# Kernel tuning notes

Measured on AMD Instinct MI355X. Metric: run time of the kernel, lower is better.

## Reference

```python
import jax, jax.numpy as jnp
import numpy as np

B, N, DIM = 2, 2048, 512
H, DH = 8, 64
INNER = H * DH
SCALE = DH ** -0.5


def setup_inputs() -> dict:
    key = jax.random.key(0)
    ks = jax.random.split(key, 8)
    s = 0.02
    return {
        "nodes": jax.random.normal(ks[0], (B, N, DIM), dtype=jnp.float32),
        "edge_mask": jax.random.bernoulli(ks[1], 0.9, (B, N, N)),
        "wq": jax.random.normal(ks[2], (DIM, INNER), dtype=jnp.float32) * s,
        "bq": jnp.zeros((INNER,), dtype=jnp.float32),
        "wkv": jax.random.normal(ks[3], (DIM, 2 * INNER), dtype=jnp.float32) * s,
        "bkv": jnp.zeros((2 * INNER,), dtype=jnp.float32),
        "wo": jax.random.normal(ks[4], (INNER, DIM), dtype=jnp.float32) * s,
        "bo": jnp.zeros((DIM,), dtype=jnp.float32),
    }


def reference(nodes, edge_mask, wq, bq, wkv, bkv, wo, bo):
    b, n, _ = nodes.shape
    q = nodes @ wq + bq                      # [b, n, h*dh]
    kv = nodes @ wkv + bkv                   # [b, n, 2*h*dh]
    k, v = jnp.split(kv, 2, axis=-1)
    # split heads -> [b, h, n, dh]
    split = lambda t: t.reshape(b, n, H, DH).transpose(0, 2, 1, 3)
    q, k, v = split(q), split(k), split(v)
    sim = jnp.einsum('bhid,bhjd->bhij', q, k) * SCALE
    max_neg = -jnp.finfo(sim.dtype).max
    sim = jnp.where(edge_mask[:, None, :, :], sim, max_neg)
    attn = jax.nn.softmax(sim, axis=-1)
    out = jnp.einsum('bhij,bhjd->bhid', attn, v)      # [b, h, n, dh]
    out = out.transpose(0, 2, 1, 3).reshape(b, n, INNER)
    return out @ wo + bo
```

## Files before the change

### kernel.cpp

```cpp
#include <hip/hip_runtime.h>
#include <cstdint>
#include <cstddef>

#define DEVI __device__ __forceinline__

typedef __bf16 bf16x8 __attribute__((ext_vector_type(8)));
typedef float floatx4 __attribute__((ext_vector_type(4)));
typedef unsigned short us4v __attribute__((ext_vector_type(4)));
typedef unsigned short us8 __attribute__((ext_vector_type(8)));

static_assert(sizeof(bf16x8) == 16, "bf16x8 must be 16B");
static_assert(sizeof(us8) == 16, "us8 must be 16B");


#if __has_builtin(__builtin_amdgcn_cvt_pk_bf16_f32)
DEVI unsigned short f2bf(float f) {
  typedef __bf16 bf16x2 __attribute__((ext_vector_type(2)));
  union { bf16x2 v; unsigned short u[2]; } c;
  c.v = __builtin_amdgcn_cvt_pk_bf16_f32(f, 0.f);
  return c.u[0];
}
#else
DEVI unsigned short f2bf(float f) {
  unsigned int u = __float_as_uint(f);
  u += 0x7fffu + ((u >> 16) & 1u);
  return (unsigned short)(u >> 16);
}
#endif

DEVI float exp2c(float x) {
#if __has_builtin(__builtin_amdgcn_exp2f)
  return __builtin_amdgcn_exp2f(x);
#else
  return exp2f(x);
#endif
}

DEVI bf16x8 ld8(const unsigned short* p) { return *(const bf16x8*)p; }

typedef const __attribute__((address_space(1))) void* gas_ptr;
typedef __attribute__((address_space(3))) void* las_ptr;

DEVI void gld16(const void* g, void* l) {
  __builtin_amdgcn_global_load_lds((gas_ptr)g, (las_ptr)l, 16, 0, 0);
}

#define WAIT_LGKM0() __builtin_amdgcn_s_waitcnt(0xc07f)
#define WAIT_VM12()  __builtin_amdgcn_s_waitcnt(0x0f7c)
#define WAIT_VM0()   __builtin_amdgcn_s_waitcnt(0x0f70)
#define SB()         __builtin_amdgcn_sched_barrier(0)

__global__ __launch_bounds__(256) void prep_k(
    const float* __restrict__ nodes, const void* __restrict__ mask,
    const float* __restrict__ wq, const float* __restrict__ wkv,
    const float* __restrict__ wo,
    unsigned short* __restrict__ XB, unsigned short* __restrict__ WQKVT,
    unsigned short* __restrict__ WOT, unsigned int* __restrict__ pm) {
  int bid = blockIdx.x;
  if (bid < 8192) {
    __shared__ int mode;
    const unsigned int* md = (const unsigned int*)mask;
    unsigned int probe = md[threadIdx.x];
    bool odd = (probe > 1u && probe != 0x3f800000u);
    if (threadIdx.x == 0) mode = 0;
    __syncthreads();
    if (odd) atomicOr(&mode, 1);
    __syncthreads();
    int byteMode = mode;
    int t = bid * 256 + threadIdx.x;
    int lane = threadIdx.x & 63;
    unsigned int n;
    if (byteMode) {
      unsigned int x = md[t];
      n = ((x & 0xffu) ? 1u : 0u) | ((x & 0xff00u) ? 2u : 0u) |
          ((x & 0xff0000u) ? 4u : 0u) | ((x >> 24) ? 8u : 0u);
    } else {
      uint4 v = ((const uint4*)mask)[t];
      n = (v.x ? 1u : 0u) | (v.y ? 2u : 0u) | (v.z ? 4u : 0u) | (v.w ? 8u : 0u);
    }
    unsigned int w = n << ((lane & 7) * 4);
    w |= __shfl_xor(w, 1);
    w |= __shfl_xor(w, 2);
    w |= __shfl_xor(w, 4);
    if ((lane & 7) == 0) pm[t >> 3] = w;
  } else if (bid < 10240) {
    int i = (bid - 8192) * 256 + threadIdx.x;
    float4 v = ((const float4*)nodes)[i];
    us4v o;
    o[0] = f2bf(v.x); o[1] = f2bf(v.y); o[2] = f2bf(v.z); o[3] = f2bf(v.w);
    *(us4v*)(XB + (size_t)i * 4) = o;
  } else {
    int tb = bid - 10240;
    int x = tb & 15, y = (tb >> 4) & 7, z = tb >> 7;
    const float* src; unsigned short* dst; int C, c0;
    if (z == 0)      { if (x >= 8) return; src = wq;  dst = WQKVT; C = 512;  c0 = 0; }
    else if (z == 1) { src = wkv; dst = WQKVT; C = 1024; c0 = 512; }
    else             { if (x >= 8) return; src = wo;  dst = WOT;  C = 512;  c0 = 0; }
    __shared__ unsigned short t2[64 * 64];
    const int t = threadIdx.x;
    const int ct = x * 64, rt = y * 64;
    for (int p = 0; p < 4; p++) {
      int kl = p * 16 + (t >> 4);
      int cc = (t & 15) * 4;
      float4 v = *(const float4*)&src[(size_t)(rt + kl) * C + ct + cc];
      float f[4] = {v.x, v.y, v.z, v.w};
      for (int i = 0; i < 4; i++) {
        int c = cc + i;
        t2[c * 64 + (kl ^ (c & 56))] = f2bf(f[i]);
      }
    }
    __syncthreads();
    for (int p = 0; p < 2; p++) {
      int c = p * 32 + (t >> 3);
      int kc = (t & 7) * 8;
      us8 v = *(const us8*)&t2[c * 64 + (kc ^ (c & 56))];
      *(us8*)&dst[(size_t)(c0 + ct + c) * 512 + rt + kc] = v;
    }
  }
}

__global__ __launch_bounds__(256) void gemm_qkv_k(
    const unsigned short* __restrict__ A,
    const unsigned short* __restrict__ Bt,
    const float* __restrict__ bq, const float* __restrict__ bkv,
    unsigned short* __restrict__ Qo, unsigned short* __restrict__ Ko,
    unsigned short* __restrict__ VTo) {
  __shared__ unsigned short smem[8192];
  unsigned short* sA = smem;
  unsigned short* sB = smem + 2048;
  const int tid = threadIdx.x;
  const int wave = tid >> 6, lane = tid & 63, quad = lane >> 4, l16 = lane & 15;
  const int wm = wave >> 1, wn = wave & 1;
  const int bm = blockIdx.x, bn = blockIdx.y;
  floatx4 acc[2][4] = {};
  const int arow = lane >> 2;
  const int ag = lane & 3;
  for (int kt = 0; kt < 16; kt++) {
    __syncthreads();
    {
      int rowA = wave * 16 + arow;
      int gA = ag ^ (rowA & 3);
      gld16(&A[(size_t)(bm * 64 + rowA) * 512 + kt * 32 + gA * 8], &sA[(wave * 16) * 32]);
      for (int p = 0; p < 2; p++) {
        int rowB = p * 64 + wave * 16 + arow;
        int gB = ag ^ (rowB & 3);
        gld16(&Bt[(size_t)(bn * 128 + rowB) * 512 + kt * 32 + gB * 8],
              &sB[(p * 64 + wave * 16) * 32]);
      }
    }
    __syncthreads();
    bf16x8 aF[2], bF[4];
    int swz = (quad ^ (l16 & 3)) * 8;
    for (int i = 0; i < 2; i++) aF[i] = ld8(&sA[(wm * 32 + i * 16 + l16) * 32 + swz]);
    for (int j = 0; j < 4; j++) bF[j] = ld8(&sB[(wn * 64 + j * 16 + l16) * 32 + swz]);
    for (int i = 0; i < 2; i++)
      for (int j = 0; j < 4; j++)
        acc[i][j] = __builtin_amdgcn_mfma_f32_16x16x32_bf16(aF[i], bF[j], acc[i][j], 0, 0, 0);
  }

  const int sec = bn * 2 + wn;
  float bias[4];
  float scale = 1.0f;
  if (sec < 8) {
    for (int j = 0; j < 4; j++) bias[j] = bq[sec * 64 + j * 16 + l16];
    scale = 0.18033688011112042f;
  } else {
    for (int j = 0; j < 4; j++) bias[j] = bkv[(sec - 8) * 64 + j * 16 + l16];
  }
  const int gr0 = bm * 64 + wm * 32;
  const int b = gr0 >> 11, n0 = gr0 & 2047;
  unsigned short* pw = smem + wave * 2048;
  __syncthreads();
  if (sec < 16) {
    for (int i = 0; i < 2; i++)
      for (int j = 0; j < 4; j++) {
        int cg = j * 2 + (l16 >> 3), ci = l16 & 7;
        for (int r = 0; r < 4; r++) {
          int row = i * 16 + quad * 4 + r;
          pw[row * 64 + ((cg ^ (row & 7)) * 8) + ci] = f2bf((acc[i][j][r] + bias[j]) * scale);
        }
      }
    WAIT_LGKM0();
    unsigned short* dst = (sec < 8) ? Qo + ((size_t)(b * 8 + sec) * 2048 + n0) * 64
                                    : Ko + ((size_t)(b * 8 + sec - 8) * 2048 + n0) * 64;
    for (int p = 0; p < 4; p++) {
      int row = p * 8 + (lane >> 3);
      int c8 = lane & 7;
      us8 v = *(const us8*)&pw[row * 64 + ((c8 ^ (row & 7)) * 8)];
      *(us8*)&dst[(size_t)row * 64 + c8 * 8] = v;
    }
  } else {
    for (int i = 0; i < 2; i++)
      for (int j = 0; j < 4; j++) {
        int d = j * 16 + l16;
        us4v t;
        for (int r = 0; r < 4; r++) t[r] = f2bf(acc[i][j][r] + bias[j]);
        *(us4v*)&pw[d * 32 + ((quad ^ (d & 3)) * 8) + i * 4] = t;
      }
    WAIT_LGKM0();
    unsigned short* dst = VTo + (size_t)(b * 8 + sec - 16) * 64 * 2048 + n0;
    for (int p = 0; p < 4; p++) {
      int d = p * 16 + (lane >> 2);
      int c4 = lane & 3;
      us8 v = *(const us8*)&pw[d * 32 + ((c4 ^ (d & 3)) * 8)];
      *(us8*)&dst[(size_t)d * 2048 + c4 * 8] = v;
    }
  }
}

__global__ __launch_bounds__(256, 2) void attn_k(
    const unsigned short* __restrict__ Q,
    const unsigned short* __restrict__ K,
    const unsigned short* __restrict__ Vt,
    const unsigned int* __restrict__ pm,
    unsigned short* __restrict__ AO) {
  __shared__ unsigned short kv[2][4][4096];
  __shared__ float lsumB[4][64];
  const int tid = threadIdx.x;
  const int wave = tid >> 6, lane = tid & 63, quad = lane >> 4, l16 = lane & 15;
  const int bh = blockIdx.x, qt = blockIdx.y, b = bh >> 3, h = bh & 7;
  const int q0 = qt * 64;
  const unsigned short* Qb = Q + (size_t)bh * 2048 * 64;
  const unsigned short* Kb = K + (size_t)bh * 2048 * 64;
  const unsigned short* Vb = Vt + (size_t)bh * 64 * 2048;
  const unsigned int* pmB = pm + (size_t)b * 2048 * 64;

  bf16x8 qF[4][2];
#pragma unroll
  for (int qb = 0; qb < 4; qb++) {
    qF[qb][0] = ld8(&Qb[(size_t)(q0 + qb * 16 + l16) * 64 + quad * 8]);
    qF[qb][1] = ld8(&Qb[(size_t)(q0 + qb * 16 + l16) * 64 + 32 + quad * 8]);
  }

  floatx4 oacc[4][4] = {};
  floatx4 lsacc[4] = {};

  union { us8 u; bf16x8 v; } onesU;
#pragma unroll
  for (int i = 0; i < 8; i++) onesU.u[i] = 0x3f80;
  const bf16x8 onesF = onesU.v;

  const int srow = lane >> 3;
  const int gK = (lane & 7) ^ srow;
  const int dV = lane >> 2;
  const int gV = (lane & 3) ^ (dV & 3);
  const int rsw0 = quad ^ (l16 & 7);
  const int rsw1 = (4 + quad) ^ (l16 & 7);

  unsigned short* kv0 = &kv[0][wave][0];
  unsigned short* kv1 = &kv[1][wave][0];

  struct MW { unsigned int w[4]; };
  MW mwA, mwB;

  auto prefetch = [&](int it, unsigned short* dst, MW& mw) {
    const int k0w = it * 128 + wave * 32;
#pragma unroll
    for (int qb = 0; qb < 4; qb++)
      mw.w[qb] = pmB[(size_t)(q0 + qb * 16 + l16) * 64 + it * 4 + wave];
#pragma unroll
    for (int p = 0; p < 4; p++) {
      gld16(&Kb[(size_t)(k0w + p * 8 + srow) * 64 + gK * 8], dst + p * 512);
      gld16(&Vb[(size_t)(p * 16 + dV) * 2048 + k0w + gV * 8], dst + 2048 + p * 512);
    }
  };

  auto step = [&](const unsigned short* buf, const MW& mw) {
    floatx4 st[4][2];
    __builtin_amdgcn_s_setprio(1);
#pragma unroll
    for (int k2 = 0; k2 < 2; k2++) {
      const unsigned short* kr = &buf[(k2 * 16 + l16) * 64];
      bf16x8 kf0 = ld8(kr + rsw0 * 8);
      bf16x8 kf1 = ld8(kr + rsw1 * 8);
#pragma unroll
      for (int qb = 0; qb < 4; qb++) {
        floatx4 z = {0.f, 0.f, 0.f, 0.f};
        z = __builtin_amdgcn_mfma_f32_16x16x32_bf16(kf0, qF[qb][0], z, 0, 0, 0);
        st[qb][k2] = __builtin_amdgcn_mfma_f32_16x16x32_bf16(kf1, qF[qb][1], z, 0, 0, 0);
      }
    }
    __builtin_amdgcn_s_setprio(0);
    union uB { bf16x8 v; unsigned short u[8]; } pf[4];
#pragma unroll
    for (int qb = 0; qb < 4; qb++) {
      unsigned int w = mw.w[qb];
#pragma unroll
      for (int k2 = 0; k2 < 2; k2++) {
#pragma unroll
        for (int r = 0; r < 4; r++) {
          float e = exp2c(st[qb][k2][r]);
          e = ((w >> (k2 * 16 + quad * 4 + r)) & 1u) ? e : 0.f;
          pf[qb].u[k2 * 4 + r] = f2bf(e);
        }
      }
    }
    __builtin_amdgcn_s_setprio(1);
#pragma unroll
    for (int qb = 0; qb < 4; qb++)
      lsacc[qb] = __builtin_amdgcn_mfma_f32_16x16x32_bf16(onesF, pf[qb].v, lsacc[qb], 0, 0, 0);
#pragma unroll
    for (int db = 0; db < 4; db++) {
      const int d = db * 16 + l16;
      bf16x8 va = ld8(&buf[2048 + d * 32 + ((quad ^ (d & 3)) * 8)]);
#pragma unroll
      for (int qb = 0; qb < 4; qb++)
        oacc[db][qb] =
            __builtin_amdgcn_mfma_f32_16x16x32_bf16(va, pf[qb].v, oacc[db][qb], 0, 0, 0);
    }
    __builtin_amdgcn_s_setprio(0);
  };

  SB();
  prefetch(0, kv0, mwA);
  SB();
#pragma unroll 1
  for (int i = 0; i < 8; ++i) {
    prefetch(i * 2 + 1, kv1, mwB);
    SB();
    WAIT_VM12();
    SB();
    step(kv0, mwA);
    SB();
    if (i < 7) {
      prefetch(i * 2 + 2, kv0, mwA);
      SB();
      WAIT_VM12();
      SB();
    } else {
      WAIT_VM0();
      SB();
    }
    step(kv1, mwB);
    SB();
  }

  if (quad == 0) {
#pragma unroll
    for (int qb = 0; qb < 4; qb++) lsumB[wave][qb * 16 + l16] = lsacc[qb][0];
  }
  __syncthreads();

  float* pO = (float*)&kv[0][0][0];
  float* myR = pO + wave * 4096;
#pragma unroll
  for (int db = 0; db < 4; db++)
#pragma unroll
    for (int qb = 0; qb < 4; qb++) {
      int q = qb * 16 + l16;
      *(floatx4*)&myR[q * 64 + (((db * 4 + quad) ^ l16) & 15) * 4] = oacc[db][qb];
    }
  __syncthreads();
  {
    int q = tid >> 2, dblk = tid & 3;
    float inv = 1.0f / (lsumB[0][q] + lsumB[1][q] + lsumB[2][q] + lsumB[3][q]);
    float o[16];
    for (int i = 0; i < 4; i++) {
      int dg = dblk * 4 + i;
      int off = q * 64 + ((dg ^ q) & 15) * 4;
      floatx4 s = *(floatx4*)&pO[off];
      s += *(floatx4*)&pO[4096 + off];
      s += *(floatx4*)&pO[8192 + off];
      s += *(floatx4*)&pO[12288 + off];
      for (int r = 0; r < 4; r++) o[i * 4 + r] = s[r] * inv;
    }
    us8 v0, v1;
    for (int i = 0; i < 8; i++) { v0[i] = f2bf(o[i]); v1[i] = f2bf(o[8 + i]); }
    unsigned short* dst = &AO[((size_t)b * 2048 + q0 + q) * 512 + h * 64 + dblk * 16];
    *(us8*)dst = v0;
    *(us8*)(dst + 8) = v1;
  }
}

__global__ __launch_bounds__(256) void gemm_out_k(
    const unsigned short* __restrict__ A,
    const unsigned short* __restrict__ Bt,
    const float* __restrict__ bo, float* __restrict__ out) {
  __shared__ unsigned short smem[6144];
  unsigned short* sA = smem;
  unsigned short* sB = smem + 2048;
  const int tid = threadIdx.x;
  const int wave = tid >> 6, lane = tid & 63, quad = lane >> 4, l16 = lane & 15;
  const int wm = wave >> 1, wn = wave & 1;
  const int bm = blockIdx.x, bn = blockIdx.y;
  floatx4 acc[2][4] = {};
  const int arow = lane >> 2;
  const int ag = lane & 3;
  for (int kt = 0; kt < 16; kt++) {
    __syncthreads();
    {
      int rowA = wave * 16 + arow;
      int gA = ag ^ (rowA & 3);
      gld16(&A[(size_t)(bm * 64 + rowA) * 512 + kt * 32 + gA * 8], &sA[(wave * 16) * 32]);
      for (int p = 0; p < 2; p++) {
        int rowB = p * 64 + wave * 16 + arow;
        int gB = ag ^ (rowB & 3);
        gld16(&Bt[(size_t)(bn * 128 + rowB) * 512 + kt * 32 + gB * 8],
              &sB[(p * 64 + wave * 16) * 32]);
      }
    }
    __syncthreads();
    bf16x8 aF[2], bF[4];
    int swz = (quad ^ (l16 & 3)) * 8;
    for (int i = 0; i < 2; i++) aF[i] = ld8(&sA[(wm * 32 + i * 16 + l16) * 32 + swz]);
    for (int j = 0; j < 4; j++) bF[j] = ld8(&sB[(wn * 64 + j * 16 + l16) * 32 + swz]);
    for (int i = 0; i < 2; i++)
      for (int j = 0; j < 4; j++)
        acc[i][j] = __builtin_amdgcn_mfma_f32_16x16x32_bf16(aF[i], bF[j], acc[i][j], 0, 0, 0);
  }
  for (int i = 0; i < 2; i++)
    for (int j = 0; j < 4; j++) {
      int gc = bn * 128 + wn * 64 + j * 16 + l16;
      float bb = bo[gc];
      for (int r = 0; r < 4; r++) {
        int gr = bm * 64 + wm * 32 + i * 16 + quad * 4 + r;
        out[(size_t)gr * 512 + gc] = acc[i][j][r] + bb;
      }
    }
}

extern "C" void kernel_launch(void* const* d_in, const int* in_sizes, int n_in,
                              void* d_out, int out_size, void* d_ws, size_t ws_size,
                              hipStream_t stream) {
  const float* nodes = (const float*)d_in[0];
  const void*  mask  = d_in[1];
  const float* wq    = (const float*)d_in[2];
  const float* bq    = (const float*)d_in[3];
  const float* wkv   = (const float*)d_in[4];
  const float* bkv   = (const float*)d_in[5];
  const float* wo    = (const float*)d_in[6];
  const float* bo    = (const float*)d_in[7];
  float* out = (float*)d_out;

  char* ws = (char*)d_ws;
  unsigned short* XB    = (unsigned short*)(ws + 0);
  unsigned short* WQKVT = (unsigned short*)(ws + 4194304);
  unsigned short* WOT   = (unsigned short*)(ws + 5767168);
  unsigned short* Qm    = (unsigned short*)(ws + 6291456);
  unsigned short* Km    = (unsigned short*)(ws + 10485760);
  unsigned short* VTm   = (unsigned short*)(ws + 18874368);
  unsigned short* AOm   = (unsigned short*)(ws + 23068672);
  unsigned int*   PM    = (unsigned int*)(ws + 27262976);

  prep_k<<<10624, 256, 0, stream>>>(nodes, mask, wq, wkv, wo, XB, WQKVT, WOT, PM);
  gemm_qkv_k<<<dim3(64, 12), 256, 0, stream>>>(XB, WQKVT, bq, bkv, Qm, Km, VTm);
  attn_k<<<dim3(16, 32), 256, 0, stream>>>(Qm, Km, VTm, PM, AOm);
  gemm_out_k<<<dim3(64, 4), 256, 0, stream>>>(AOm, WOT, bo, out);
}
```

Baseline: 152.5 us.

## Fuse all four stages into one persistent kernel with grid barriers

Replaces the four separate launches (prep, QKV GEMM, attention, output GEMM) with a single persistent 512-block kernel. Each stage is processed with a grid-stride loop over the old block indices, and stages are separated by atomic-counter grid barriers, with a memset zeroing the counter beforehand. This is meant to remove launch gaps and per-kernel tail effects. In exchange it relies on all 512 blocks being co-resident (two per CU at 65KB of shared memory each), adds spin-wait barrier cost, and leaves some blocks idle in the output-GEMM stage.

```diff
diff --git a/kernel.cpp b/kernel.cpp
--- a/kernel.cpp
+++ b/kernel.cpp
@@ -50,373 +50,386 @@
 #define WAIT_VM0()   __builtin_amdgcn_s_waitcnt(0x0f70)
 #define SB()         __builtin_amdgcn_sched_barrier(0)
 
-__global__ __launch_bounds__(256) void prep_k(
+DEVI void grid_bar(unsigned int* cnt, unsigned int target, int tid) {
+  __syncthreads();
+  if (tid == 0) {
+    __threadfence();
+    __hip_atomic_fetch_add(cnt, 1u, __ATOMIC_ACQ_REL, __HIP_MEMORY_SCOPE_AGENT);
+    while (__hip_atomic_load(cnt, __ATOMIC_ACQUIRE, __HIP_MEMORY_SCOPE_AGENT) < target)
+      __builtin_amdgcn_s_sleep(16);
+  }
+  __syncthreads();
+}
+
+__global__ __launch_bounds__(256, 2) void mega_k(
     const float* __restrict__ nodes, const void* __restrict__ mask,
     const float* __restrict__ wq, const float* __restrict__ wkv,
     const float* __restrict__ wo,
+    const float* __restrict__ bq, const float* __restrict__ bkv,
+    const float* __restrict__ bo,
     unsigned short* __restrict__ XB, unsigned short* __restrict__ WQKVT,
-    unsigned short* __restrict__ WOT, unsigned int* __restrict__ pm) {
-  int bid = blockIdx.x;
-  if (bid < 8192) {
-    __shared__ int mode;
-    const unsigned int* md = (const unsigned int*)mask;
-    unsigned int probe = md[threadIdx.x];
-    bool odd = (probe > 1u && probe != 0x3f800000u);
-    if (threadIdx.x == 0) mode = 0;
-    __syncthreads();
-    if (odd) atomicOr(&mode, 1);
-    __syncthreads();
-    int byteMode = mode;
-    int t = bid * 256 + threadIdx.x;
-    int lane = threadIdx.x & 63;
-    unsigned int n;
-    if (byteMode) {
-      unsigned int x = md[t];
-      n = ((x & 0xffu) ? 1u : 0u) | ((x & 0xff00u) ? 2u : 0u) |
-          ((x & 0xff0000u) ? 4u : 0u) | ((x >> 24) ? 8u : 0u);
-    } else {
-      uint4 v = ((const uint4*)mask)[t];
-      n = (v.x ? 1u : 0u) | (v.y ? 2u : 0u) | (v.z ? 4u : 0u) | (v.w ? 8u : 0u);
-    }
-    unsigned int w = n << ((lane & 7) * 4);
-    w |= __shfl_xor(w, 1);
-    w |= __shfl_xor(w, 2);
-    w |= __shfl_xor(w, 4);
-    if ((lane & 7) == 0) pm[t >> 3] = w;
-  } else if (bid < 10240) {
-    int i = (bid - 8192) * 256 + threadIdx.x;
-    float4 v = ((const float4*)nodes)[i];
-    us4v o;
-    o[0] = f2bf(v.x); o[1] = f2bf(v.y); o[2] = f2bf(v.z); o[3] = f2bf(v.w);
-    *(us4v*)(XB + (size_t)i * 4) = o;
-  } else {
-    int tb = bid - 10240;
-    int x = tb & 15, y = (tb >> 4) & 7, z = tb >> 7;
-    const float* src; unsigned short* dst; int C, c0;
-    if (z == 0)      { if (x >= 8) return; src = wq;  dst = WQKVT; C = 512;  c0 = 0; }
-    else if (z == 1) { src = wkv; dst = WQKVT; C = 1024; c0 = 512; }
-    else             { if (x >= 8) return; src = wo;  dst = WOT;  C = 512;  c0 = 0; }
-    __shared__ unsigned short t2[64 * 64];
-    const int t = threadIdx.x;
-    const int ct = x * 64, rt = y * 64;
-    for (int p = 0; p < 4; p++) {
-      int kl = p * 16 + (t >> 4);
-      int cc = (t & 15) * 4;
-      float4 v = *(const float4*)&src[(size_t)(rt + kl) * C + ct + cc];
-      float f[4] = {v.x, v.y, v.z, v.w};
-      for (int i = 0; i < 4; i++) {
-        int c = cc + i;
-        t2[c * 64 + (kl ^ (c & 56))] = f2bf(f[i]);
-      }
-    }
-    __syncthreads();
-    for (int p = 0; p < 2; p++) {
-      int c = p * 32 + (t >> 3);
-      int kc = (t & 7) * 8;
-      us8 v = *(const us8*)&t2[c * 64 + (kc ^ (c & 56))];
-      *(us8*)&dst[(size_t)(c0 + ct + c) * 512 + rt + kc] = v;
-    }
-  }
-}
-
-__global__ __launch_bounds__(256) void gemm_qkv_k(
-    const unsigned short* __restrict__ A,
-    const unsigned short* __restrict__ Bt,
-    const float* __restrict__ bq, const float* __restrict__ bkv,
-    unsigned short* __restrict__ Qo, unsigned short* __restrict__ Ko,
-    unsigned short* __restrict__ VTo) {
-  __shared__ unsigned short smem[8192];
-  unsigned short* sA = smem;
-  unsigned short* sB = smem + 2048;
+    unsigned short* __restrict__ WOT, unsigned int* __restrict__ pm,
+    unsigned short* __restrict__ Qm, unsigned short* __restrict__ Km,
+    unsigned short* __restrict__ VTm, unsigned short* __restrict__ AOm,
+    float* __restrict__ out, unsigned int* __restrict__ gcnt) {
+  __shared__ alignas(16) char smU[66560];
+  const int blk = blockIdx.x;
   const int tid = threadIdx.x;
   const int wave = tid >> 6, lane = tid & 63, quad = lane >> 4, l16 = lane & 15;
-  const int wm = wave >> 1, wn = wave & 1;
-  const int bm = blockIdx.x, bn = blockIdx.y;
-  floatx4 acc[2][4] = {};
-  const int arow = lane >> 2;
-  const int ag = lane & 3;
-  for (int kt = 0; kt < 16; kt++) {
-    __syncthreads();
-    {
-      int rowA = wave * 16 + arow;
-      int gA = ag ^ (rowA & 3);
-      gld16(&A[(size_t)(bm * 64 + rowA) * 512 + kt * 32 + gA * 8], &sA[(wave * 16) * 32]);
-      for (int p = 0; p < 2; p++) {
-        int rowB = p * 64 + wave * 16 + arow;
-        int gB = ag ^ (rowB & 3);
-        gld16(&Bt[(size_t)(bn * 128 + rowB) * 512 + kt * 32 + gB * 8],
-              &sB[(p * 64 + wave * 16) * 32]);
-      }
-    }
-    __syncthreads();
-    bf16x8 aF[2], bF[4];
-    int swz = (quad ^ (l16 & 3)) * 8;
-    for (int i = 0; i < 2; i++) aF[i] = ld8(&sA[(wm * 32 + i * 16 + l16) * 32 + swz]);
-    for (int j = 0; j < 4; j++) bF[j] = ld8(&sB[(wn * 64 + j * 16 + l16) * 32 + swz]);
-    for (int i = 0; i < 2; i++)
-      for (int j = 0; j < 4; j++)
-        acc[i][j] = __builtin_amdgcn_mfma_f32_16x16x32_bf16(aF[i], bF[j], acc[i][j], 0, 0, 0);
+
+  {
+    int* modeP = (int*)(smU + 65536);
+    unsigned short* t2 = (unsigned short*)smU;
+    for (int bid = blk; bid < 10624; bid += 512) {
+      __syncthreads();
+      if (bid < 8192) {
+        const unsigned int* md = (const unsigned int*)mask;
+        unsigned int probe = md[tid];
+        bool odd = (probe > 1u && probe != 0x3f800000u);
+        if (tid == 0) *modeP = 0;
+        __syncthreads();
+        if (odd) atomicOr(modeP, 1);
+        __syncthreads();
+        int byteMode = *modeP;
+        int t = bid * 256 + tid;
+        unsigned int n;
+        if (byteMode) {
+          unsigned int x = md[t];
+          n = ((x & 0xffu) ? 1u : 0u) | ((x & 0xff00u) ? 2u : 0u) |
+              ((x & 0xff0000u) ? 4u : 0u) | ((x >> 24) ? 8u : 0u);
+        } else {
+          uint4 v = ((const uint4*)mask)[t];
+          n = (v.x ? 1u : 0u) | (v.y ? 2u : 0u) | (v.z ? 4u : 0u) | (v.w ? 8u : 0u);
+        }
+        unsigned int w = n << ((lane & 7) * 4);
+        w |= __shfl_xor(w, 1);
+        w |= __shfl_xor(w, 2);
+        w |= __shfl_xor(w, 4);
+        if ((lane & 7) == 0) pm[t >> 3] = w;
+      } else if (bid < 10240) {
+        int i = (bid - 8192) * 256 + tid;
+        float4 v = ((const float4*)nodes)[i];
+        us4v o;
+        o[0] = f2bf(v.x); o[1] = f2bf(v.y); o[2] = f2bf(v.z); o[3] = f2bf(v.w);
+        *(us4v*)(XB + (size_t)i * 4) = o;
+      } else {
+        int tb = bid - 10240;
+        int x = tb & 15, y = (tb >> 4) & 7, z = tb >> 7;
+        const float* src; unsigned short* dst; int C, c0;
+        bool active = true;
+        if (z == 0)      { if (x >= 8) active = false; src = wq;  dst = WQKVT; C = 512;  c0 = 0; }
+        else if (z == 1) { src = wkv; dst = WQKVT; C = 1024; c0 = 512; }
+        else             { if (x >= 8) active = false; src = wo;  dst = WOT;  C = 512;  c0 = 0; }
+        if (active) {
+          const int t = tid;
+          const int ct = x * 64, rt = y * 64;
+          for (int p = 0; p < 4; p++) {
+            int kl = p * 16 + (t >> 4);
+            int cc = (t & 15) * 4;
+            float4 v = *(const float4*)&src[(size_t)(rt + kl) * C + ct + cc];
+            float f[4] = {v.x, v.y, v.z, v.w};
+            for (int i = 0; i < 4; i++) {
+              int c = cc + i;
+              t2[c * 64 + (kl ^ (c & 56))] = f2bf(f[i]);
+            }
+          }
+          __syncthreads();
+          for (int p = 0; p < 2; p++) {
+            int c = p * 32 + (t >> 3);
+            int kc = (t & 7) * 8;
+            us8 v = *(const us8*)&t2[c * 64 + (kc ^ (c & 56))];
+            *(us8*)&dst[(size_t)(c0 + ct + c) * 512 + rt + kc] = v;
+          }
+        }
+      }
+    }
   }
-
-  const int sec = bn * 2 + wn;
-  float bias[4];
-  float scale = 1.0f;
-  if (sec < 8) {
-    for (int j = 0; j < 4; j++) bias[j] = bq[sec * 64 + j * 16 + l16];
-    scale = 0.18033688011112042f;
-  } else {
-    for (int j = 0; j < 4; j++) bias[j] = bkv[(sec - 8) * 64 + j * 16 + l16];
+  grid_bar(gcnt, 512, tid);
+
+  {
+    unsigned short* smem = (unsigned short*)smU;
+    unsigned short* sA = smem;
+    unsigned short* sB = smem + 2048;
+    const int wm = wave >> 1, wn = wave & 1;
+    const int arow = lane >> 2;
+    const int ag = lane & 3;
+    for (int t = blk; t < 768; t += 512) {
+      const int bm = t & 63, bn = t >> 6;
+      floatx4 acc[2][4] = {};
+      for (int kt = 0; kt < 16; kt++) {
+        __syncthreads();
+        {
+          int rowA = wave * 16 + arow;
+          int gA = ag ^ (rowA & 3);
+          gld16(&XB[(size_t)(bm * 64 + rowA) * 512 + kt * 32 + gA * 8], &sA[(wave * 16) * 32]);
+          for (int p = 0; p < 2; p++) {
+            int rowB = p * 64 + wave * 16 + arow;
+            int gB = ag ^ (rowB & 3);
+            gld16(&WQKVT[(size_t)(bn * 128 + rowB) * 512 + kt * 32 + gB * 8],
+                  &sB[(p * 64 + wave * 16) * 32]);
+          }
+        }
+        __syncthreads();
+        bf16x8 aF[2], bF[4];
+        int swz = (quad ^ (l16 & 3)) * 8;
+        for (int i = 0; i < 2; i++) aF[i] = ld8(&sA[(wm * 32 + i * 16 + l16) * 32 + swz]);
+        for (int j = 0; j < 4; j++) bF[j] = ld8(&sB[(wn * 64 + j * 16 + l16) * 32 + swz]);
+        for (int i = 0; i < 2; i++)
+          for (int j = 0; j < 4; j++)
+            acc[i][j] = __builtin_amdgcn_mfma_f32_16x16x32_bf16(aF[i], bF[j], acc[i][j], 0, 0, 0);
+      }
+
+      const int sec = bn * 2 + wn;
+      float bias[4];
+      float scale = 1.0f;
+      if (sec < 8) {
+        for (int j = 0; j < 4; j++) bias[j] = bq[sec * 64 + j * 16 + l16];
+        scale = 0.18033688011112042f;
+      } else {
+        for (int j = 0; j < 4; j++) bias[j] = bkv[(sec - 8) * 64 + j * 16 + l16];
+      }
+      const int gr0 = bm * 64 + wm * 32;
+      const int b = gr0 >> 11, n0 = gr0 & 2047;
+      unsigned short* pw = smem + wave * 2048;
+      __syncthreads();
+      if (sec < 16) {
+        for (int i = 0; i < 2; i++)
+          for (int j = 0; j < 4; j++) {
+            int cg2 = j * 2 + (l16 >> 3), ci = l16 & 7;
+            for (int r = 0; r < 4; r++) {
+              int row = i * 16 + quad * 4 + r;
+              pw[row * 64 + ((cg2 ^ (row & 7)) * 8) + ci] = f2bf((acc[i][j][r] + bias[j]) * scale);
+            }
+          }
+        WAIT_LGKM0();
+        unsigned short* dst = (sec < 8) ? Qm + ((size_t)(b * 8 + sec) * 2048 + n0) * 64
+                                        : Km + ((size_t)(b * 8 + sec - 8) * 2048 + n0) * 64;
+        for (int p = 0; p < 4; p++) {
+          int row = p * 8 + (lane >> 3);
+          int c8 = lane & 7;
+          us8 v = *(const us8*)&pw[row * 64 + ((c8 ^ (row & 7)) * 8)];
+          *(us8*)&dst[(size_t)row * 64 + c8 * 8] = v;
+        }
+      } else {
+        for (int i = 0; i < 2; i++)
+          for (int j = 0; j < 4; j++) {
+            int d = j * 16 + l16;
+            us4v tv;
+            for (int r = 0; r < 4; r++) tv[r] = f2bf(acc[i][j][r] + bias[j]);
+            *(us4v*)&pw[d * 32 + ((quad ^ (d & 3)) * 8) + i * 4] = tv;
+          }
+        WAIT_LGKM0();
+        unsigned short* dst = VTm + (size_t)(b * 8 + sec - 16) * 64 * 2048 + n0;
+        for (int p = 0; p < 4; p++) {
+          int d = p * 16 + (lane >> 2);
+          int c4 = lane & 3;
+          us8 v = *(const us8*)&pw[d * 32 + ((c4 ^ (d & 3)) * 8)];
+          *(us8*)&dst[(size_t)d * 2048 + c4 * 8] = v;
+        }
+      }
+    }
   }
-  const int gr0 = bm * 64 + wm * 32;
-  const int b = gr0 >> 11, n0 = gr0 & 2047;
-  unsigned short* pw = smem + wave * 2048;
-  __syncthreads();
-  if (sec < 16) {
-    for (int i = 0; i < 2; i++)
-      for (int j = 0; j < 4; j++) {
-        int cg = j * 2 + (l16 >> 3), ci = l16 & 7;
-        for (int r = 0; r < 4; r++) {
-          int row = i * 16 + quad * 4 + r;
-          pw[row * 64 + ((cg ^ (row & 7)) * 8) + ci] = f2bf((acc[i][j][r] + bias[j]) * scale);
-        }
-      }
-    WAIT_LGKM0();
-    unsigned short* dst = (sec < 8) ? Qo + ((size_t)(b * 8 + sec) * 2048 + n0) * 64
-                                    : Ko + ((size_t)(b * 8 + sec - 8) * 2048 + n0) * 64;
-    for (int p = 0; p < 4; p++) {
-      int row = p * 8 + (lane >> 3);
-      int c8 = lane & 7;
-      us8 v = *(const us8*)&pw[row * 64 + ((c8 ^ (row & 7)) * 8)];
-      *(us8*)&dst[(size_t)row * 64 + c8 * 8] = v;
-    }
-  } else {
-    for (int i = 0; i < 2; i++)
-      for (int j = 0; j < 4; j++) {
-        int d = j * 16 + l16;
-        us4v t;
-        for (int r = 0; r < 4; r++) t[r] = f2bf(acc[i][j][r] + bias[j]);
-        *(us4v*)&pw[d * 32 + ((quad ^ (d & 3)) * 8) + i * 4] = t;
-      }
-    WAIT_LGKM0();
-    unsigned short* dst = VTo + (size_t)(b * 8 + sec - 16) * 64 * 2048 + n0;
-    for (int p = 0; p < 4; p++) {
-      int d = p * 16 + (lane >> 2);
-      int c4 = lane & 3;
-      us8 v = *(const us8*)&pw[d * 32 + ((c4 ^ (d & 3)) * 8)];
-      *(us8*)&dst[(size_t)d * 2048 + c4 * 8] = v;
-    }
-  }
-}
-
-__global__ __launch_bounds__(256, 2) void attn_k(
-    const unsigned short* __restrict__ Q,
-    const unsigned short* __restrict__ K,
-    const unsigned short* __restrict__ Vt,
-    const unsigned int* __restrict__ pm,
-    unsigned short* __restrict__ AO) {
-  __shared__ unsigned short kv[2][4][4096];
-  __shared__ float lsumB[4][64];
-  const int tid = threadIdx.x;
-  const int wave = tid >> 6, lane = tid & 63, quad = lane >> 4, l16 = lane & 15;
-  const int bh = blockIdx.x, qt = blockIdx.y, b = bh >> 3, h = bh & 7;
-  const int q0 = qt * 64;
-  const unsigned short* Qb = Q + (size_t)bh * 2048 * 64;
-  const unsigned short* Kb = K + (size_t)bh * 2048 * 64;
-  const unsigned short* Vb = Vt + (size_t)bh * 64 * 2048;
-  const unsigned int* pmB = pm + (size_t)b * 2048 * 64;
-
-  bf16x8 qF[4][2];
-#pragma unroll
-  for (int qb = 0; qb < 4; qb++) {
-    qF[qb][0] = ld8(&Qb[(size_t)(q0 + qb * 16 + l16) * 64 + quad * 8]);
-    qF[qb][1] = ld8(&Qb[(size_t)(q0 + qb * 16 + l16) * 64 + 32 + quad * 8]);
-  }
-
-  floatx4 oacc[4][4] = {};
-  floatx4 lsacc[4] = {};
-
-  union { us8 u; bf16x8 v; } onesU;
-#pragma unroll
-  for (int i = 0; i < 8; i++) onesU.u[i] = 0x3f80;
-  const bf16x8 onesF = onesU.v;
-
-  const int srow = lane >> 3;
-  const int gK = (lane & 7) ^ srow;
-  const int dV = lane >> 2;
-  const int gV = (lane & 3) ^ (dV & 3);
-  const int rsw0 = quad ^ (l16 & 7);
-  const int rsw1 = (4 + quad) ^ (l16 & 7);
-
-  unsigned short* kv0 = &kv[0][wave][0];
-  unsigned short* kv1 = &kv[1][wave][0];
-
-  struct MW { unsigned int w[4]; };
-  MW mwA, mwB;
-
-  auto prefetch = [&](int it, unsigned short* dst, MW& mw) {
-    const int k0w = it * 128 + wave * 32;
-#pragma unroll
-    for (int qb = 0; qb < 4; qb++)
-      mw.w[qb] = pmB[(size_t)(q0 + qb * 16 + l16) * 64 + it * 4 + wave];
-#pragma unroll
-    for (int p = 0; p < 4; p++) {
-      gld16(&Kb[(size_t)(k0w + p * 8 + srow) * 64 + gK * 8], dst + p * 512);
-      gld16(&Vb[(size_t)(p * 16 + dV) * 2048 + k0w + gV * 8], dst + 2048 + p * 512);
-    }
-  };
-
-  auto step = [&](const unsigned short* buf, const MW& mw) {
-    floatx4 st[4][2];
-    __builtin_amdgcn_s_setprio(1);
-#pragma unroll
-    for (int k2 = 0; k2 < 2; k2++) {
-      const unsigned short* kr = &buf[(k2 * 16 + l16) * 64];
-      bf16x8 kf0 = ld8(kr + rsw0 * 8);
-      bf16x8 kf1 = ld8(kr + rsw1 * 8);
+  grid_bar(gcnt, 1024, tid);
+
+  {
+    unsigned short (*kv)[4][4096] = (unsigned short (*)[4][4096])smU;
+    float (*lsumB)[64] = (float (*)[64])(smU + 65536);
+    const int bh = blk & 15, qt = blk >> 4, b = bh >> 3, h = bh & 7;
+    const int q0 = qt * 64;
+    const unsigned short* Qb = Qm + (size_t)bh * 2048 * 64;
+    const unsigned short* Kb = Km + (size_t)bh * 2048 * 64;
+    const unsigned short* Vb = VTm + (size_t)bh * 64 * 2048;
+    const unsigned int* pmB = pm + (size_t)b * 2048 * 64;
+
+    bf16x8 qF[4][2];
+#pragma unroll
+    for (int qb = 0; qb < 4; qb++) {
+      qF[qb][0] = ld8(&Qb[(size_t)(q0 + qb * 16 + l16) * 64 + quad * 8]);
+      qF[qb][1] = ld8(&Qb[(size_t)(q0 + qb * 16 + l16) * 64 + 32 + quad * 8]);
+    }
+
+    floatx4 oacc[4][4] = {};
+    floatx4 lsacc[4] = {};
+
+    union { us8 u; bf16x8 v; } onesU;
+#pragma unroll
+    for (int i = 0; i < 8; i++) onesU.u[i] = 0x3f80;
+    const bf16x8 onesF = onesU.v;
+
+    const int srow = lane >> 3;
+    const int gK = (lane & 7) ^ srow;
+    const int dV = lane >> 2;
+    const int gV = (lane & 3) ^ (dV & 3);
+    const int rsw0 = quad ^ (l16 & 7);
+    const int rsw1 = (4 + quad) ^ (l16 & 7);
+
+    unsigned short* kv0 = &kv[0][wave][0];
+    unsigned short* kv1 = &kv[1][wave][0];
+
+    struct MW { unsigned int w[4]; };
+    MW mwA, mwB;
+
+    auto prefetch = [&](int it, unsigned short* dst, MW& mw) {
+      const int k0w = it * 128 + wave * 32;
+#pragma unroll
+      for (int qb = 0; qb < 4; qb++)
+        mw.w[qb] = pmB[(size_t)(q0 + qb * 16 + l16) * 64 + it * 4 + wave];
+#pragma unroll
+      for (int p = 0; p < 4; p++) {
+        gld16(&Kb[(size_t)(k0w + p * 8 + srow) * 64 + gK * 8], dst + p * 512);
+        gld16(&Vb[(size_t)(p * 16 + dV) * 2048 + k0w + gV * 8], dst + 2048 + p * 512);
+      }
+    };
+
+    auto step = [&](const unsigned short* buf, const MW& mw) {
+      floatx4 st[4][2];
+      __builtin_amdgcn_s_setprio(1);
+#pragma unroll
+      for (int k2 = 0; k2 < 2; k2++) {
+        const unsigned short* kr = &buf[(k2 * 16 + l16) * 64];
+        bf16x8 kf0 = ld8(kr + rsw0 * 8);
+        bf16x8 kf1 = ld8(kr + rsw1 * 8);
+#pragma unroll
+        for (int qb = 0; qb < 4; qb++) {
+          floatx4 z = {0.f, 0.f, 0.f, 0.f};
+          z = __builtin_amdgcn_mfma_f32_16x16x32_bf16(kf0, qF[qb][0], z, 0, 0, 0);
+          st[qb][k2] = __builtin_amdgcn_mfma_f32_16x16x32_bf16(kf1, qF[qb][1], z, 0, 0, 0);
+        }
+      }
+      __builtin_amdgcn_s_setprio(0);
+      union uB { bf16x8 v; unsigned short u[8]; } pf[4];
 #pragma unroll
       for (int qb = 0; qb < 4; qb++) {
-        floatx4 z = {0.f, 0.f, 0.f, 0.f};
-        z = __builtin_amdgcn_mfma_f32_16x16x32_bf16(kf0, qF[qb][0], z, 0, 0, 0);
-        st[qb][k2] = __builtin_amdgcn_mfma_f32_16x16x32_bf16(kf1, qF[qb][1], z, 0, 0, 0);
-      }
-    }
-    __builtin_amdgcn_s_setprio(0);
-    union uB { bf16x8 v; unsigned short u[8]; } pf[4];
-#pragma unroll
-    for (int qb = 0; qb < 4; qb++) {
-      unsigned int w = mw.w[qb];
-#pragma unroll
-      for (int k2 = 0; k2 < 2; k2++) {
-#pragma unroll
-        for (int r = 0; r < 4; r++) {
-          float e = exp2c(st[qb][k2][r]);
-          e = ((w >> (k2 * 16 + quad * 4 + r)) & 1u) ? e : 0.f;
-          pf[qb].u[k2 * 4 + r] = f2bf(e);
-        }
-      }
-    }
-    __builtin_amdgcn_s_setprio(1);
-#pragma unroll
-    for (int qb = 0; qb < 4; qb++)
-      lsacc[qb] = __builtin_amdgcn_mfma_f32_16x16x32_bf16(onesF, pf[qb].v, lsacc[qb], 0, 0, 0);
-#pragma unroll
-    for (int db = 0; db < 4; db++) {
-      const int d = db * 16 + l16;
-      bf16x8 va = ld8(&buf[2048 + d * 32 + ((quad ^ (d & 3)) * 8)]);
+        unsigned int w = mw.w[qb];
+#pragma unroll
+        for (int k2 = 0; k2 < 2; k2++) {
+#pragma unroll
+          for (int r = 0; r < 4; r++) {
+            float e = exp2c(st[qb][k2][r]);
+            e = ((w >> (k2 * 16 + quad * 4 + r)) & 1u) ? e : 0.f;
+            pf[qb].u[k2 * 4 + r] = f2bf(e);
+          }
+        }
+      }
+      __builtin_amdgcn_s_setprio(1);
 #pragma unroll
       for (int qb = 0; qb < 4; qb++)
-        oacc[db][qb] =
-            __builtin_amdgcn_mfma_f32_16x16x32_bf16(va, pf[qb].v, oacc[db][qb], 0, 0, 0);
-    }
-    __builtin_amdgcn_s_setprio(0);
-  };
-
-  SB();
-  prefetch(0, kv0, mwA);
-  SB();
+        lsacc[qb] = __builtin_amdgcn_mfma_f32_16x16x32_bf16(onesF, pf[qb].v, lsacc[qb], 0, 0, 0);
+#pragma unroll
+      for (int db = 0; db < 4; db++) {
+        const int d = db * 16 + l16;
+        bf16x8 va = ld8(&buf[2048 + d * 32 + ((quad ^ (d & 3)) * 8)]);
+#pragma unroll
+        for (int qb = 0; qb < 4; qb++)
+          oacc[db][qb] =
+              __builtin_amdgcn_mfma_f32_16x16x32_bf16(va, pf[qb].v, oacc[db][qb], 0, 0, 0);
+      }
+      __builtin_amdgcn_s_setprio(0);
+    };
+
+    SB();
+    prefetch(0, kv0, mwA);
+    SB();
 #pragma unroll 1
-  for (int i = 0; i < 8; ++i) {
-    prefetch(i * 2 + 1, kv1, mwB);
-    SB();
-    WAIT_VM12();
-    SB();
-    step(kv0, mwA);
-    SB();
-    if (i < 7) {
-      prefetch(i * 2 + 2, kv0, mwA);
+    for (int i = 0; i < 8; ++i) {
+      prefetch(i * 2 + 1, kv1, mwB);
       SB();
       WAIT_VM12();
       SB();
-    } else {
-      WAIT_VM0();
+      step(kv0, mwA);
       SB();
-    }
-    step(kv1, mwB);
-    SB();
-  }
-
-  if (quad == 0) {
-#pragma unroll
-    for (int qb = 0; qb < 4; qb++) lsumB[wave][qb * 16 + l16] = lsacc[qb][0];
-  }
-  __syncthreads();
-
-  float* pO = (float*)&kv[0][0][0];
-  float* myR = pO + wave * 4096;
-#pragma unroll
-  for (int db = 0; db < 4; db++)
-#pragma unroll
-    for (int qb = 0; qb < 4; qb++) {
-      int q = qb * 16 + l16;
-      *(floatx4*)&myR[q * 64 + (((db * 4 + quad) ^ l16) & 15) * 4] = oacc[db][qb];
-    }
-  __syncthreads();
-  {
-    int q = tid >> 2, dblk = tid & 3;
-    float inv = 1.0f / (lsumB[0][q] + lsumB[1][q] + lsumB[2][q] + lsumB[3][q]);
-    float o[16];
-    for (int i = 0; i < 4; i++) {
-      int dg = dblk * 4 + i;
-      int off = q * 64 + ((dg ^ q) & 15) * 4;
-      floatx4 s = *(floatx4*)&pO[off];
-      s += *(floatx4*)&pO[4096 + off];
-      s += *(floatx4*)&pO[8192 + off];
-      s += *(floatx4*)&pO[12288 + off];
-      for (int r = 0; r < 4; r++) o[i * 4 + r] = s[r] * inv;
-    }
-    us8 v0, v1;
-    for (int i = 0; i < 8; i++) { v0[i] = f2bf(o[i]); v1[i] = f2bf(o[8 + i]); }
-    unsigned short* dst = &AO[((size_t)b * 2048 + q0 + q) * 512 + h * 64 + dblk * 16];
-    *(us8*)dst = v0;
-    *(us8*)(dst + 8) = v1;
-  }
-}
-
-__global__ __launch_bounds__(256) void gemm_out_k(
-    const unsigned short* __restrict__ A,
-    const unsigned short* __restrict__ Bt,
-    const float* __restrict__ bo, float* __restrict__ out) {
-  __shared__ unsigned short smem[6144];
-  unsigned short* sA = smem;
-  unsigned short* sB = smem + 2048;
-  const int tid = threadIdx.x;
-  const int wave = tid >> 6, lane = tid & 63, quad = lane >> 4, l16 = lane & 15;
-  const int wm = wave >> 1, wn = wave & 1;
-  const int bm = blockIdx.x, bn = blockIdx.y;
-  floatx4 acc[2][4] = {};
-  const int arow = lane >> 2;
-  const int ag = lane & 3;
-  for (int kt = 0; kt < 16; kt++) {
+      if (i < 7) {
+        prefetch(i * 2 + 2, kv0, mwA);
+        SB();
+        WAIT_VM12();
+        SB();
+      } else {
+        WAIT_VM0();
+        SB();
+      }
+      step(kv1, mwB);
+      SB();
+    }
+
+    if (quad == 0) {
+#pragma unroll
+      for (int qb = 0; qb < 4; qb++) lsumB[wave][qb * 16 + l16] = lsacc[qb][0];
+    }
+    __syncthreads();
+
+    float* pO = (float*)smU;
+    float* myR = pO + wave * 4096;
+#pragma unroll
+    for (int db = 0; db < 4; db++)
+#pragma unroll
+      for (int qb = 0; qb < 4; qb++) {
+        int q = qb * 16 + l16;
+        *(floatx4*)&myR[q * 64 + (((db * 4 + quad) ^ l16) & 15) * 4] = oacc[db][qb];
+      }
     __syncthreads();
     {
-      int rowA = wave * 16 + arow;
-      int gA = ag ^ (rowA & 3);
-      gld16(&A[(size_t)(bm * 64 + rowA) * 512 + kt * 32 + gA * 8], &sA[(wave * 16) * 32]);
-      for (int p = 0; p < 2; p++) {
-        int rowB = p * 64 + wave * 16 + arow;
-        int gB = ag ^ (rowB & 3);
-        gld16(&Bt[(size_t)(bn * 128 + rowB) * 512 + kt * 32 + gB * 8],
-              &sB[(p * 64 + wave * 16) * 32]);
-      }
-    }
-    __syncthreads();
-    bf16x8 aF[2], bF[4];
-    int swz = (quad ^ (l16 & 3)) * 8;
-    for (int i = 0; i < 2; i++) aF[i] = ld8(&sA[(wm * 32 + i * 16 + l16) * 32 + swz]);
-    for (int j = 0; j < 4; j++) bF[j] = ld8(&sB[(wn * 64 + j * 16 + l16) * 32 + swz]);
+      int q = tid >> 2, dblk = tid & 3;
+      float inv = 1.0f / (lsumB[0][q] + lsumB[1][q] + lsumB[2][q] + lsumB[3][q]);
+      float o[16];
+      for (int i = 0; i < 4; i++) {
+        int dg = dblk * 4 + i;
+        int off = q * 64 + ((dg ^ q) & 15) * 4;
+        floatx4 s = *(floatx4*)&pO[off];
+        s += *(floatx4*)&pO[4096 + off];
+        s += *(floatx4*)&pO[8192 + off];
+        s += *(floatx4*)&pO[12288 + off];
+        for (int r = 0; r < 4; r++) o[i * 4 + r] = s[r] * inv;
+      }
+      us8 v0, v1;
+      for (int i = 0; i < 8; i++) { v0[i] = f2bf(o[i]); v1[i] = f2bf(o[8 + i]); }
+      unsigned short* dst = &AOm[((size_t)b * 2048 + q0 + q) * 512 + h * 64 + dblk * 16];
+      *(us8*)dst = v0;
+      *(us8*)(dst + 8) = v1;
+    }
+  }
+  grid_bar(gcnt, 1536, tid);
+
+  if (blk < 256) {
+    unsigned short* smem = (unsigned short*)smU;
+    unsigned short* sA = smem;
+    unsigned short* sB = smem + 2048;
+    const int wm = wave >> 1, wn = wave & 1;
+    const int bm = blk & 63, bn = blk >> 6;
+    floatx4 acc[2][4] = {};
+    const int arow = lane >> 2;
+    const int ag = lane & 3;
+    for (int kt = 0; kt < 16; kt++) {
+      __syncthreads();
+      {
+        int rowA = wave * 16 + arow;
+        int gA = ag ^ (rowA & 3);
+        gld16(&AOm[(size_t)(bm * 64 + rowA) * 512 + kt * 32 + gA * 8], &sA[(wave * 16) * 32]);
+        for (int p = 0; p < 2; p++) {
+          int rowB = p * 64 + wave * 16 + arow;
+          int gB = ag ^ (rowB & 3);
+          gld16(&WOT[(size_t)(bn * 128 + rowB) * 512 + kt * 32 + gB * 8],
+                &sB[(p * 64 + wave * 16) * 32]);
+        }
+      }
+      __syncthreads();
+      bf16x8 aF[2], bF[4];
+      int swz = (quad ^ (l16 & 3)) * 8;
+      for (int i = 0; i < 2; i++) aF[i] = ld8(&sA[(wm * 32 + i * 16 + l16) * 32 + swz]);
+      for (int j = 0; j < 4; j++) bF[j] = ld8(&sB[(wn * 64 + j * 16 + l16) * 32 + swz]);
+      for (int i = 0; i < 2; i++)
+        for (int j = 0; j < 4; j++)
+          acc[i][j] = __builtin_amdgcn_mfma_f32_16x16x32_bf16(aF[i], bF[j], acc[i][j], 0, 0, 0);
+    }
     for (int i = 0; i < 2; i++)
-      for (int j = 0; j < 4; j++)
-        acc[i][j] = __builtin_amdgcn_mfma_f32_16x16x32_bf16(aF[i], bF[j], acc[i][j], 0, 0, 0);
+      for (int j = 0; j < 4; j++) {
+        int gc = bn * 128 + wn * 64 + j * 16 + l16;
+        float bb = bo[gc];
+        for (int r = 0; r < 4; r++) {
+          int gr = bm * 64 + wm * 32 + i * 16 + quad * 4 + r;
+          out[(size_t)gr * 512 + gc] = acc[i][j][r] + bb;
+        }
+      }
   }
-  for (int i = 0; i < 2; i++)
-    for (int j = 0; j < 4; j++) {
-      int gc = bn * 128 + wn * 64 + j * 16 + l16;
-      float bb = bo[gc];
-      for (int r = 0; r < 4; r++) {
-        int gr = bm * 64 + wm * 32 + i * 16 + quad * 4 + r;
-        out[(size_t)gr * 512 + gc] = acc[i][j][r] + bb;
-      }
-    }
 }
 
 extern "C" void kernel_launch(void* const* d_in, const int* in_sizes, int n_in,
@@ -441,9 +454,9 @@
   unsigned short* VTm   = (unsigned short*)(ws + 18874368);
   unsigned short* AOm   = (unsigned short*)(ws + 23068672);
   unsigned int*   PM    = (unsigned int*)(ws + 27262976);
-
-  prep_k<<<10624, 256, 0, stream>>>(nodes, mask, wq, wkv, wo, XB, WQKVT, WOT, PM);
-  gemm_qkv_k<<<dim3(64, 12), 256, 0, stream>>>(XB, WQKVT, bq, bkv, Qm, Km, VTm);
-  attn_k<<<dim3(16, 32), 256, 0, stream>>>(Qm, Km, VTm, PM, AOm);
-  gemm_out_k<<<dim3(64, 4), 256, 0, stream>>>(AOm, WOT, bo, out);
-}
+  unsigned int*   CNT   = (unsigned int*)(ws + 28311552);
+
+  hipMemsetAsync(CNT, 0, 128, stream);
+  mega_k<<<512, 256, 0, stream>>>(nodes, mask, wq, wkv, wo, bq, bkv, bo,
+                                  XB, WQKVT, WOT, PM, Qm, Km, VTm, AOm, out, CNT);
+}
```

Result: slower. 396.8 us (+160.2%).

## Fuse output projection into attention kernel via per-tile cross-head counter barrier

Applied to the files above, without the earlier changes.

The attention kernel now writes its bf16 per-head output with agent-scope stores. It then bumps a per-(batch, query-tile) counter and spins until all 8 head blocks for that tile have arrived. Each block then computes a 64x64 slice of the output projection for its head's column range, which removes the separate gemm_out launch. This trades one kernel launch and a tail gap for a global spin barrier that assumes all 8 head blocks are co-resident. It also adds a memset and slower uncached loads of the attention output.

```diff
diff --git a/kernel.cpp b/kernel.cpp
--- a/kernel.cpp
+++ b/kernel.cpp
@@ -49,6 +49,13 @@
 #define WAIT_VM12()  __builtin_amdgcn_s_waitcnt(0x0f7c)
 #define WAIT_VM0()   __builtin_amdgcn_s_waitcnt(0x0f70)
 #define SB()         __builtin_amdgcn_sched_barrier(0)
+
+DEVI void st8_sc1(unsigned long long* p, unsigned long long v) {
+  __hip_atomic_store(p, v, __ATOMIC_RELAXED, __HIP_MEMORY_SCOPE_AGENT);
+}
+DEVI unsigned long long ld8_sc1(const unsigned long long* p) {
+  return __hip_atomic_load(p, __ATOMIC_RELAXED, __HIP_MEMORY_SCOPE_AGENT);
+}
 
 __global__ __launch_bounds__(256) void prep_k(
     const float* __restrict__ nodes, const void* __restrict__ mask,
@@ -208,12 +215,15 @@
   }
 }
 
-__global__ __launch_bounds__(256, 2) void attn_k(
+__global__ __launch_bounds__(256, 2) void attn_out_k(
     const unsigned short* __restrict__ Q,
     const unsigned short* __restrict__ K,
     const unsigned short* __restrict__ Vt,
     const unsigned int* __restrict__ pm,
-    unsigned short* __restrict__ AO) {
+    unsigned short* __restrict__ AO,
+    const unsigned short* __restrict__ Bt,
+    const float* __restrict__ bo, float* __restrict__ out,
+    unsigned int* __restrict__ tcnt) {
   __shared__ unsigned short kv[2][4][4096];
   __shared__ float lsumB[4][64];
   const int tid = threadIdx.x;
@@ -364,59 +374,69 @@
       s += *(floatx4*)&pO[12288 + off];
       for (int r = 0; r < 4; r++) o[i * 4 + r] = s[r] * inv;
     }
-    us8 v0, v1;
-    for (int i = 0; i < 8; i++) { v0[i] = f2bf(o[i]); v1[i] = f2bf(o[8 + i]); }
-    unsigned short* dst = &AO[((size_t)b * 2048 + q0 + q) * 512 + h * 64 + dblk * 16];
-    *(us8*)dst = v0;
-    *(us8*)(dst + 8) = v1;
-  }
-}
-
-__global__ __launch_bounds__(256) void gemm_out_k(
-    const unsigned short* __restrict__ A,
-    const unsigned short* __restrict__ Bt,
-    const float* __restrict__ bo, float* __restrict__ out) {
-  __shared__ unsigned short smem[6144];
-  unsigned short* sA = smem;
-  unsigned short* sB = smem + 2048;
-  const int tid = threadIdx.x;
-  const int wave = tid >> 6, lane = tid & 63, quad = lane >> 4, l16 = lane & 15;
-  const int wm = wave >> 1, wn = wave & 1;
-  const int bm = blockIdx.x, bn = blockIdx.y;
-  floatx4 acc[2][4] = {};
-  const int arow = lane >> 2;
-  const int ag = lane & 3;
-  for (int kt = 0; kt < 16; kt++) {
-    __syncthreads();
-    {
-      int rowA = wave * 16 + arow;
-      int gA = ag ^ (rowA & 3);
-      gld16(&A[(size_t)(bm * 64 + rowA) * 512 + kt * 32 + gA * 8], &sA[(wave * 16) * 32]);
-      for (int p = 0; p < 2; p++) {
-        int rowB = p * 64 + wave * 16 + arow;
-        int gB = ag ^ (rowB & 3);
-        gld16(&Bt[(size_t)(bn * 128 + rowB) * 512 + kt * 32 + gB * 8],
-              &sB[(p * 64 + wave * 16) * 32]);
-      }
-    }
-    __syncthreads();
-    bf16x8 aF[2], bF[4];
-    int swz = (quad ^ (l16 & 3)) * 8;
-    for (int i = 0; i < 2; i++) aF[i] = ld8(&sA[(wm * 32 + i * 16 + l16) * 32 + swz]);
-    for (int j = 0; j < 4; j++) bF[j] = ld8(&sB[(wn * 64 + j * 16 + l16) * 32 + swz]);
+    union { us8 v; unsigned long long q2[2]; } v0, v1;
+    for (int i = 0; i < 8; i++) { v0.v[i] = f2bf(o[i]); v1.v[i] = f2bf(o[8 + i]); }
+    unsigned long long* dst =
+        (unsigned long long*)&AO[((size_t)b * 2048 + q0 + q) * 512 + h * 64 + dblk * 16];
+    st8_sc1(dst + 0, v0.q2[0]);
+    st8_sc1(dst + 1, v0.q2[1]);
+    st8_sc1(dst + 2, v1.q2[0]);
+    st8_sc1(dst + 3, v1.q2[1]);
+  }
+
+  WAIT_VM0();
+  __syncthreads();
+  if (tid == 0) {
+    __hip_atomic_fetch_add(&tcnt[b * 32 + qt], 1u,
+                           __ATOMIC_RELAXED, __HIP_MEMORY_SCOPE_AGENT);
+    while (__hip_atomic_load(&tcnt[b * 32 + qt],
+                             __ATOMIC_RELAXED, __HIP_MEMORY_SCOPE_AGENT) < 8u)
+      __builtin_amdgcn_s_sleep(16);
+  }
+  __syncthreads();
+
+  {
+    unsigned short* sA = &kv[0][0][0];
+    unsigned short* sB = sA + 2048;
+    const int wm = wave >> 1, wn = wave & 1;
+    const int bmrow = b * 2048 + qt * 64;
+    const int arow = tid >> 2;
+    const int ag4 = tid & 3;
+    const int gA = ag4 ^ (arow & 3);
+    const int browB = wave * 16 + (lane >> 2);
+    const int gB = (lane & 3) ^ (browB & 3);
+    floatx4 acc[2][2] = {};
+    for (int kt = 0; kt < 16; kt++) {
+      __syncthreads();
+      {
+        const unsigned long long* src = (const unsigned long long*)
+            &AO[(size_t)(bmrow + arow) * 512 + kt * 32 + gA * 8];
+        unsigned long long x0 = ld8_sc1(src);
+        unsigned long long x1 = ld8_sc1(src + 1);
+        unsigned long long* d = (unsigned long long*)&sA[arow * 32 + ag4 * 8];
+        d[0] = x0; d[1] = x1;
+        gld16(&Bt[(size_t)(h * 64 + browB) * 512 + kt * 32 + gB * 8],
+              &sB[(wave * 16) * 32]);
+      }
+      __syncthreads();
+      bf16x8 aF[2], bF[2];
+      int swz = (quad ^ (l16 & 3)) * 8;
+      for (int i = 0; i < 2; i++) aF[i] = ld8(&sA[(wm * 32 + i * 16 + l16) * 32 + swz]);
+      for (int j = 0; j < 2; j++) bF[j] = ld8(&sB[(wn * 32 + j * 16 + l16) * 32 + swz]);
+      for (int i = 0; i < 2; i++)
+        for (int j = 0; j < 2; j++)
+          acc[i][j] = __builtin_amdgcn_mfma_f32_16x16x32_bf16(aF[i], bF[j], acc[i][j], 0, 0, 0);
+    }
     for (int i = 0; i < 2; i++)
-      for (int j = 0; j < 4; j++)
-        acc[i][j] = __builtin_amdgcn_mfma_f32_16x16x32_bf16(aF[i], bF[j], acc[i][j], 0, 0, 0);
-  }
-  for (int i = 0; i < 2; i++)
-    for (int j = 0; j < 4; j++) {
-      int gc = bn * 128 + wn * 64 + j * 16 + l16;
-      float bb = bo[gc];
-      for (int r = 0; r < 4; r++) {
-        int gr = bm * 64 + wm * 32 + i * 16 + quad * 4 + r;
-        out[(size_t)gr * 512 + gc] = acc[i][j][r] + bb;
-      }
-    }
+      for (int j = 0; j < 2; j++) {
+        int gc = h * 64 + wn * 32 + j * 16 + l16;
+        float bb = bo[gc];
+        for (int r = 0; r < 4; r++) {
+          int gr = bmrow + wm * 32 + i * 16 + quad * 4 + r;
+          out[(size_t)gr * 512 + gc] = acc[i][j][r] + bb;
+        }
+      }
+  }
 }
 
 extern "C" void kernel_launch(void* const* d_in, const int* in_sizes, int n_in,
@@ -441,9 +461,10 @@
   unsigned short* VTm   = (unsigned short*)(ws + 18874368);
   unsigned short* AOm   = (unsigned short*)(ws + 23068672);
   unsigned int*   PM    = (unsigned int*)(ws + 27262976);
-
+  unsigned int*   CNT   = (unsigned int*)(ws + 28311552);
+
+  hipMemsetAsync(CNT, 0, 512, stream);
   prep_k<<<10624, 256, 0, stream>>>(nodes, mask, wq, wkv, wo, XB, WQKVT, WOT, PM);
   gemm_qkv_k<<<dim3(64, 12), 256, 0, stream>>>(XB, WQKVT, bq, bkv, Qm, Km, VTm);
-  attn_k<<<dim3(16, 32), 256, 0, stream>>>(Qm, Km, VTm, PM, AOm);
-  gemm_out_k<<<dim3(64, 4), 256, 0, stream>>>(AOm, WOT, bo, out);
-}
+  attn_out_k<<<dim3(16, 32), 256, 0, stream>>>(Qm, Km, VTm, PM, AOm, WOT, bo, out, CNT);
+}
```

New measurement: 170.8 us. +12.0%, slower.
